# Performance work log

Measured on AMD Instinct MI355X. Metric: run time of the kernel, lower is better.

The kernel has to match this reference:

```python
import jax, jax.numpy as jnp
import numpy as np

NUM_SITES = 64
PHYS_DIM = 2
BOND_DIM = 32
BATCH = 65536


def _build_mps(num_sites, phys_dim, bond_dim, seed=0):
    """Replicates ImprovedMPS._initialize_tensors + _canonical_form, then
    zero-pads ragged cores into a dense [S, D, p, D] stack."""
    rng = np.random.default_rng(seed)
    tensors = []
    cur = 1
    for i in range(num_sites):
        if i == 0:
            nb = min(bond_dim, phys_dim)
            shape = (1, phys_dim, nb)
            cur = nb
        elif i == num_sites - 1:
            shape = (cur, phys_dim, 1)
        else:
            nb = min(bond_dim, cur * phys_dim)
            shape = (cur, phys_dim, nb)
            cur = nb
        ld, rd = shape[0] * shape[1], shape[2]
        m = (rng.standard_normal((ld, rd)) * 0.1).astype(np.float32)
        if ld >= rd:
            q, _ = np.linalg.qr(m)
            t = q.reshape(shape)
        else:
            q, _ = np.linalg.qr(m.T)
            t = q.T.reshape(shape)
        tensors.append(t.astype(np.float32))
    # left-canonical sweep
    for i in range(num_sites - 1):
        l, p, r = tensors[i].shape
        q, rr = np.linalg.qr(tensors[i].reshape(l * p, r))
        tensors[i] = q.reshape(l, p, q.shape[1]).astype(np.float32)
        nl, npd, nr = tensors[i + 1].shape
        tensors[i + 1] = (rr @ tensors[i + 1].reshape(nl, npd * nr)).reshape(rr.shape[0], npd, nr).astype(np.float32)
    # zero-pad ragged bonds into dense stack [S, D, p, D]
    A = np.zeros((num_sites, bond_dim, phys_dim, bond_dim), dtype=np.float32)
    for i, t in enumerate(tensors):
        l, p, r = t.shape
        A[i, :l, :, :r] = t
    return A


def setup_inputs() -> dict:
    key = jax.random.key(0)
    x_batch = jax.random.normal(key, (BATCH, NUM_SITES, PHYS_DIM), dtype=jnp.float32)
    A = jnp.asarray(_build_mps(NUM_SITES, PHYS_DIM, BOND_DIM))
    return {"x_batch": x_batch, "A": A}


def reference(x_batch, A):
    # x_batch: [B, S, p]; A: [S, D, p, D] (zero-padded ragged MPS cores)
    B = x_batch.shape[0]
    D = A.shape[1]
    # left_vector starts as ones(B,1) in the ragged view == one-hot e0 in padded view
    left0 = jnp.zeros((B, D), dtype=x_batch.dtype).at[:, 0].set(1.0)
    xs = jnp.moveaxis(x_batch, 1, 0)  # [S, B, p]

    def step(left, inp):
        A_i, x_i = inp  # [D, p, D], [B, p]
        # fuses: contracted = einsum('bp,lpd->bld'); left = einsum('bl,bld->bd')
        left = jnp.einsum('bl,bp,lpd->bd', left, x_i, A_i)
        return left, None

    left, _ = jax.lax.scan(step, left0, (A, xs))
    return left[:, :1]  # last core has right bond 1 -> only col 0 is nonzero
```

## Files before the change

kernel.cpp:

```cpp
#include <hip/hip_runtime.h>


typedef _Float16 h2 __attribute__((ext_vector_type(2)));
typedef _Float16 half8 __attribute__((ext_vector_type(8)));
typedef float floatx4 __attribute__((ext_vector_type(4)));
typedef float f32x4 __attribute__((ext_vector_type(4)));

#define NPAIRS 32
#define CHUNK_ELEMS 16384

__global__ void mps_prep_pair(const float* __restrict__ A, _Float16* __restrict__ Gf) {
    __shared__ float sA0[2048], sA1[2048], sG[4096];
    const int P = blockIdx.x, tid = threadIdx.x;
    const float* a0p = A + (size_t)(2 * P) * 2048;
    const float* a1p = A + (size_t)(2 * P + 1) * 2048;
#pragma unroll
    for (int i = 0; i < 8; ++i) {
        sA0[tid + 256 * i] = a0p[tid + 256 * i];
        sA1[tid + 256 * i] = a1p[tid + 256 * i];
    }
    __syncthreads();
    {
        const int l = tid >> 3, pq = (tid >> 1) & 3, dh16 = (tid & 1) * 16;
        const int p = pq >> 1, q = pq & 1;
        float accv[16];
#pragma unroll
        for (int dd = 0; dd < 16; ++dd) accv[dd] = 0.f;
        for (int m = 0; m < 32; ++m) {
            const float av = sA0[l * 64 + p * 32 + m];
            const float* bp = &sA1[m * 64 + q * 32 + dh16];
#pragma unroll
            for (int dd = 0; dd < 16; ++dd) accv[dd] += av * bp[dd];
        }
#pragma unroll
        for (int dd = 0; dd < 16; ++dd) sG[l * 128 + pq * 32 + dh16 + dd] = accv[dd];
    }
    __syncthreads();
    const int lane = tid & 63, g = lane >> 4;
#pragma unroll
    for (int pass = 0; pass < 2; ++pass) {
        const int fr = (tid >> 6) + pass * 4;
        const int dh = fr >> 2, kh = fr & 3;
        const int d  = 16 * dh + (lane & 15);
        half8 v;
#pragma unroll
        for (int e = 0; e < 8; ++e) {
            const int l = 4 * g + (e & 3) + 16 * (e >> 2);
            v[e] = (_Float16)sG[l * 128 + kh * 32 + d];
        }
        reinterpret_cast<half8*>(Gf)[((size_t)P * 8 + fr) * 64 + lane] = v;
    }
}

static __device__ __forceinline__ half8 H8(h2 a, h2 b, h2 c, h2 d) {
    half8 r;
    r[0] = a[0]; r[1] = a[1]; r[2] = b[0]; r[3] = b[1];
    r[4] = c[0]; r[5] = c[1]; r[6] = d[0]; r[7] = d[1];
    return r;
}

#define MF(A_, B_, C_) __builtin_amdgcn_mfma_f32_16x16x32_f16(A_, B_, C_, 0, 0, 0)

#define UB(U0, U1, U2, U3, AH0, AH1, XV)                                      \
    {                                                                         \
        h2 b0, b1, b2, b3, w0, w1, w2, w3;                                    \
        b0[0] = (_Float16)AH0[0]; b0[1] = (_Float16)AH0[1];                   \
        b1[0] = (_Float16)AH0[2]; b1[1] = (_Float16)AH0[3];                   \
        b2[0] = (_Float16)AH1[0]; b2[1] = (_Float16)AH1[1];                   \
        b3[0] = (_Float16)AH1[2]; b3[1] = (_Float16)AH1[3];                   \
        _Float16 t_;                                                          \
        t_ = (_Float16)(XV[0] * XV[2]); w0[0] = t_; w0[1] = t_;               \
        t_ = (_Float16)(XV[0] * XV[3]); w1[0] = t_; w1[1] = t_;               \
        t_ = (_Float16)(XV[1] * XV[2]); w2[0] = t_; w2[1] = t_;               \
        t_ = (_Float16)(XV[1] * XV[3]); w3[0] = t_; w3[1] = t_;               \
        U0 = H8(b0 * w0, b1 * w0, b2 * w0, b3 * w0);                          \
        U1 = H8(b0 * w1, b1 * w1, b2 * w1, b3 * w1);                          \
        U2 = H8(b0 * w2, b1 * w2, b2 * w2, b3 * w2);                          \
        U3 = H8(b0 * w3, b1 * w3, b2 * w3, b3 * w3);                          \
    }

#define PAIR(G, I00, I01, I10, I11, O00, O01, O10, O11, XV0, XV1)             \
    {                                                                         \
        half8 u0_, u1_, u2_, u3_, v0_, v1_, v2_, v3_;                         \
        UB(u0_, u1_, u2_, u3_, I00, I01, XV0)                                 \
        UB(v0_, v1_, v2_, v3_, I10, I11, XV1)                                 \
        O00 = MF(G[0], u0_, zv);  O01 = MF(G[4], u0_, zv);                    \
        O10 = MF(G[0], v0_, zv);  O11 = MF(G[4], v0_, zv);                    \
        O00 = MF(G[1], u1_, O00); O01 = MF(G[5], u1_, O01);                   \
        O10 = MF(G[1], v1_, O10); O11 = MF(G[5], v1_, O11);                   \
        O00 = MF(G[2], u2_, O00); O01 = MF(G[6], u2_, O01);                   \
        O10 = MF(G[2], v2_, O10); O11 = MF(G[6], v2_, O11);                   \
        O00 = MF(G[3], u3_, O00); O01 = MF(G[7], u3_, O01);                   \
        O10 = MF(G[3], v3_, O10); O11 = MF(G[7], v3_, O11);                   \
    }

#define RD(DST, BUF, PL)                                                      \
    {                                                                         \
        _Pragma("unroll")                                                     \
        for (int f_ = 0; f_ < 8; ++f_)                                        \
            DST[f_] = *(const half8*)&smA[(BUF) * CHUNK_ELEMS                 \
                                          + (((PL) * 8 + f_) * 64 + lane) * 8]; \
    }

#define STAGE(C, BUF)                                                         \
    {                                                                         \
        _Pragma("unroll")                                                     \
        for (int r_ = 0; r_ < 8; ++r_) {                                      \
            const int rec_ = r_ * 4 + wid;                                    \
            const _Float16* g_ = Gf + (size_t)(C) * CHUNK_ELEMS               \
                                 + rec_ * 512 + lane * 8;                     \
            __builtin_amdgcn_global_load_lds(                                 \
                (const __attribute__((address_space(1))) void*)g_,            \
                (__attribute__((address_space(3))) void*)&smA[(BUF) * CHUNK_ELEMS + rec_ * 512], \
                16, 0, 0);                                                    \
        }                                                                     \
    }

#define CHUNKB(C, BUF, XC0, XC1, XN0, XN1)                                    \
    {                                                                         \
        if ((C) < 7) {                                                        \
            STAGE((C) + 1, 1 - (BUF));                                        \
            _Pragma("unroll")                                                 \
            for (int pp_ = 0; pp_ < 4; ++pp_) {                               \
                XN0[pp_] = xp0[4 * ((C) + 1) + pp_];                          \
                XN1[pp_] = xp1[4 * ((C) + 1) + pp_];                          \
            }                                                                 \
        }                                                                     \
        RD(GB, BUF, 1)                                                        \
        PAIR(GA, p0, p1, q0, q1, np0, np1, nq0, nq1, XC0[0], XC1[0])          \
        RD(GA, BUF, 2)                                                        \
        PAIR(GB, np0, np1, nq0, nq1, p0, p1, q0, q1, XC0[1], XC1[1])          \
        RD(GB, BUF, 3)                                                        \
        PAIR(GA, p0, p1, q0, q1, np0, np1, nq0, nq1, XC0[2], XC1[2])          \
        PAIR(GB, np0, np1, nq0, nq1, p0, p1, q0, q1, XC0[3], XC1[3])          \
        __syncthreads();                                                      \
        if ((C) < 7) RD(GA, 1 - (BUF), 0)                                     \
    }

__global__ __launch_bounds__(256, 2) void mps_main(const float* __restrict__ x,
                                                   const _Float16* __restrict__ Gf,
                                                   float* __restrict__ out) {
    __shared__ __align__(16) _Float16 smA[2 * CHUNK_ELEMS];

    const int lane  = threadIdx.x & 63;
    const int wid   = threadIdx.x >> 6;
    const int wbase = (blockIdx.x * 4 + wid) * 32;
    const int r     = lane & 15;
    const int b0    = wbase + r;
    const int b1    = wbase + 16 + r;

    const f32x4* xp0 = reinterpret_cast<const f32x4*>(x + (size_t)b0 * 128);
    const f32x4* xp1 = reinterpret_cast<const f32x4*>(x + (size_t)b1 * 128);

    floatx4 zv;
#pragma unroll
    for (int i = 0; i < 4; ++i) zv[i] = 0.f;

    floatx4 p0, p1, q0, q1, np0, np1, nq0, nq1;
#pragma unroll
    for (int i = 0; i < 4; ++i) {
        p0[i] = 0.f; p1[i] = 0.f; q0[i] = 0.f; q1[i] = 0.f;
        np0[i] = 0.f; np1[i] = 0.f; nq0[i] = 0.f; nq1[i] = 0.f;
    }
    if (lane < 16) { p0[0] = 1.f; q0[0] = 1.f; }

    f32x4 xa0[4], xa1[4], xb0[4], xb1[4];
    half8 GA[8], GB[8];

    STAGE(0, 0);
#pragma unroll
    for (int pp = 0; pp < 4; ++pp) { xa0[pp] = xp0[pp]; xa1[pp] = xp1[pp]; }
    __syncthreads();
    RD(GA, 0, 0)

    for (int it = 0; it < 4; ++it) {
        const int c0 = 2 * it;
        CHUNKB(c0,     0, xa0, xa1, xb0, xb1)
        CHUNKB(c0 + 1, 1, xb0, xb1, xa0, xa1)
    }

    if (lane < 16) {
        out[wbase + lane]      = p0[0];
        out[wbase + 16 + lane] = q0[0];
    }
}

extern "C" void kernel_launch(void* const* d_in, const int* in_sizes, int n_in,
                              void* d_out, int out_size, void* d_ws, size_t ws_size,
                              hipStream_t stream) {
    const float* x = (const float*)d_in[0];
    const float* A = (const float*)d_in[1];
    float* outp = (float*)d_out;
    _Float16* Gf = (_Float16*)d_ws;

    hipLaunchKernelGGL(mps_prep_pair, dim3(NPAIRS), dim3(256), 0, stream, A, Gf);
    hipLaunchKernelGGL(mps_main, dim3(65536 / 128), dim3(256), 0, stream, x, Gf, outp);
}
```

Baseline: 31.87 us.

## Process four 16-sample tiles per wave with two-wave blocks

```diff
diff --git a/kernel.cpp b/kernel.cpp
--- a/kernel.cpp
+++ b/kernel.cpp
@@ -39,16 +39,24 @@
     const int lane = tid & 63, g = lane >> 4;
 #pragma unroll
     for (int pass = 0; pass < 2; ++pass) {
-        const int fr = (tid >> 6) + pass * 4;
-        const int dh = fr >> 2, kh = fr & 3;
-        const int d  = 16 * dh + (lane & 15);
-        half8 v;
-#pragma unroll
-        for (int e = 0; e < 8; ++e) {
-            const int l = 4 * g + (e & 3) + 16 * (e >> 2);
-            v[e] = (_Float16)sG[l * 128 + kh * 32 + d];
+        const int fr = (tid >> 6) + pass * 2;
+        (void)fr;
+    }
+    {
+        const int lane2 = tid & 63, g2 = lane2 >> 4;
+#pragma unroll
+        for (int pass = 0; pass < 2; ++pass) {
+            const int fr = (tid >> 6) + pass * 4;
+            const int dh = fr >> 2, kh = fr & 3;
+            const int d  = 16 * dh + (lane2 & 15);
+            half8 v;
+#pragma unroll
+            for (int e = 0; e < 8; ++e) {
+                const int l = 4 * g2 + (e & 3) + 16 * (e >> 2);
+                v[e] = (_Float16)sG[l * 128 + kh * 32 + d];
+            }
+            reinterpret_cast<half8*>(Gf)[((size_t)P * 8 + fr) * 64 + lane2] = v;
         }
-        reinterpret_cast<half8*>(Gf)[((size_t)P * 8 + fr) * 64 + lane] = v;
     }
 }
 
@@ -79,20 +87,26 @@
         U3 = H8(b0 * w3, b1 * w3, b2 * w3, b3 * w3);                          \
     }
 
-#define PAIR(G, I00, I01, I10, I11, O00, O01, O10, O11, XV0, XV1)             \
-    {                                                                         \
-        half8 u0_, u1_, u2_, u3_, v0_, v1_, v2_, v3_;                         \
-        UB(u0_, u1_, u2_, u3_, I00, I01, XV0)                                 \
-        UB(v0_, v1_, v2_, v3_, I10, I11, XV1)                                 \
-        O00 = MF(G[0], u0_, zv);  O01 = MF(G[4], u0_, zv);                    \
-        O10 = MF(G[0], v0_, zv);  O11 = MF(G[4], v0_, zv);                    \
-        O00 = MF(G[1], u1_, O00); O01 = MF(G[5], u1_, O01);                   \
-        O10 = MF(G[1], v1_, O10); O11 = MF(G[5], v1_, O11);                   \
-        O00 = MF(G[2], u2_, O00); O01 = MF(G[6], u2_, O01);                   \
-        O10 = MF(G[2], v2_, O10); O11 = MF(G[6], v2_, O11);                   \
-        O00 = MF(G[3], u3_, O00); O01 = MF(G[7], u3_, O01);                   \
-        O10 = MF(G[3], v3_, O10); O11 = MF(G[7], v3_, O11);                   \
-    }
+#define PAIR1(G, I0, I1, O0, O1, XV)                                          \
+    {                                                                         \
+        half8 u0_, u1_, u2_, u3_;                                             \
+        UB(u0_, u1_, u2_, u3_, I0, I1, XV)                                    \
+        O0 = MF(G[0], u0_, zv);  O1 = MF(G[4], u0_, zv);                      \
+        O0 = MF(G[1], u1_, O0);  O1 = MF(G[5], u1_, O1);                      \
+        O0 = MF(G[2], u2_, O0);  O1 = MF(G[6], u2_, O1);                      \
+        O0 = MF(G[3], u3_, O0);  O1 = MF(G[7], u3_, O1);                      \
+    }
+
+#define PAIR4_E(G, XC, PP)                                                    \
+    PAIR1(G, a0h0, a0h1, n0h0, n0h1, XC[0][PP])                               \
+    PAIR1(G, a1h0, a1h1, n1h0, n1h1, XC[1][PP])                               \
+    PAIR1(G, a2h0, a2h1, n2h0, n2h1, XC[2][PP])                               \
+    PAIR1(G, a3h0, a3h1, n3h0, n3h1, XC[3][PP])
+#define PAIR4_O(G, XC, PP)                                                    \
+    PAIR1(G, n0h0, n0h1, a0h0, a0h1, XC[0][PP])                               \
+    PAIR1(G, n1h0, n1h1, a1h0, a1h1, XC[1][PP])                               \
+    PAIR1(G, n2h0, n2h1, a2h0, a2h1, XC[2][PP])                               \
+    PAIR1(G, n3h0, n3h1, a3h0, a3h1, XC[3][PP])
 
 #define RD(DST, BUF, PL)                                                      \
     {                                                                         \
@@ -105,8 +119,8 @@
 #define STAGE(C, BUF)                                                         \
     {                                                                         \
         _Pragma("unroll")                                                     \
-        for (int r_ = 0; r_ < 8; ++r_) {                                      \
-            const int rec_ = r_ * 4 + wid;                                    \
+        for (int r_ = 0; r_ < 16; ++r_) {                                     \
+            const int rec_ = r_ * 2 + wid;                                    \
             const _Float16* g_ = Gf + (size_t)(C) * CHUNK_ELEMS               \
                                  + rec_ * 512 + lane * 8;                     \
             __builtin_amdgcn_global_load_lds(                                 \
@@ -116,72 +130,82 @@
         }                                                                     \
     }
 
-#define CHUNKB(C, BUF, XC0, XC1, XN0, XN1)                                    \
+#define CHUNKB(C, BUF, XC, XN)                                                \
     {                                                                         \
         if ((C) < 7) {                                                        \
             STAGE((C) + 1, 1 - (BUF));                                        \
             _Pragma("unroll")                                                 \
-            for (int pp_ = 0; pp_ < 4; ++pp_) {                               \
-                XN0[pp_] = xp0[4 * ((C) + 1) + pp_];                          \
-                XN1[pp_] = xp1[4 * ((C) + 1) + pp_];                          \
-            }                                                                 \
+            for (int tt_ = 0; tt_ < 4; ++tt_)                                 \
+                _Pragma("unroll")                                             \
+                for (int pp_ = 0; pp_ < 4; ++pp_)                             \
+                    XN[tt_][pp_] = xp[tt_][4 * ((C) + 1) + pp_];              \
         }                                                                     \
         RD(GB, BUF, 1)                                                        \
-        PAIR(GA, p0, p1, q0, q1, np0, np1, nq0, nq1, XC0[0], XC1[0])          \
+        PAIR4_E(GA, XC, 0)                                                    \
         RD(GA, BUF, 2)                                                        \
-        PAIR(GB, np0, np1, nq0, nq1, p0, p1, q0, q1, XC0[1], XC1[1])          \
+        PAIR4_O(GB, XC, 1)                                                    \
         RD(GB, BUF, 3)                                                        \
-        PAIR(GA, p0, p1, q0, q1, np0, np1, nq0, nq1, XC0[2], XC1[2])          \
-        PAIR(GB, np0, np1, nq0, nq1, p0, p1, q0, q1, XC0[3], XC1[3])          \
+        PAIR4_E(GA, XC, 2)                                                    \
+        PAIR4_O(GB, XC, 3)                                                    \
         __syncthreads();                                                      \
         if ((C) < 7) RD(GA, 1 - (BUF), 0)                                     \
     }
 
-__global__ __launch_bounds__(256, 2) void mps_main(const float* __restrict__ x,
+__global__ __launch_bounds__(128, 1) void mps_main(const float* __restrict__ x,
                                                    const _Float16* __restrict__ Gf,
                                                    float* __restrict__ out) {
     __shared__ __align__(16) _Float16 smA[2 * CHUNK_ELEMS];
 
     const int lane  = threadIdx.x & 63;
     const int wid   = threadIdx.x >> 6;
-    const int wbase = (blockIdx.x * 4 + wid) * 32;
+    const int wbase = (blockIdx.x * 2 + wid) * 64;
     const int r     = lane & 15;
-    const int b0    = wbase + r;
-    const int b1    = wbase + 16 + r;
-
-    const f32x4* xp0 = reinterpret_cast<const f32x4*>(x + (size_t)b0 * 128);
-    const f32x4* xp1 = reinterpret_cast<const f32x4*>(x + (size_t)b1 * 128);
+
+    const f32x4* xp[4];
+#pragma unroll
+    for (int tt = 0; tt < 4; ++tt)
+        xp[tt] = reinterpret_cast<const f32x4*>(x + (size_t)(wbase + 16 * tt + r) * 128);
 
     floatx4 zv;
 #pragma unroll
     for (int i = 0; i < 4; ++i) zv[i] = 0.f;
 
-    floatx4 p0, p1, q0, q1, np0, np1, nq0, nq1;
+    floatx4 a0h0, a0h1, a1h0, a1h1, a2h0, a2h1, a3h0, a3h1;
+    floatx4 n0h0, n0h1, n1h0, n1h1, n2h0, n2h1, n3h0, n3h1;
 #pragma unroll
     for (int i = 0; i < 4; ++i) {
-        p0[i] = 0.f; p1[i] = 0.f; q0[i] = 0.f; q1[i] = 0.f;
-        np0[i] = 0.f; np1[i] = 0.f; nq0[i] = 0.f; nq1[i] = 0.f;
-    }
-    if (lane < 16) { p0[0] = 1.f; q0[0] = 1.f; }
-
-    f32x4 xa0[4], xa1[4], xb0[4], xb1[4];
+        a0h0[i] = a0h1[i] = a1h0[i] = a1h1[i] = 0.f;
+        a2h0[i] = a2h1[i] = a3h0[i] = a3h1[i] = 0.f;
+        n0h0[i] = n0h1[i] = n1h0[i] = n1h1[i] = 0.f;
+        n2h0[i] = n2h1[i] = n3h0[i] = n3h1[i] = 0.f;
+    }
+    if (lane < 16) { a0h0[0] = 1.f; a1h0[0] = 1.f; a2h0[0] = 1.f; a3h0[0] = 1.f; }
+
+    f32x4 xa[4][4], xb[4][4];
     half8 GA[8], GB[8];
 
     STAGE(0, 0);
 #pragma unroll
-    for (int pp = 0; pp < 4; ++pp) { xa0[pp] = xp0[pp]; xa1[pp] = xp1[pp]; }
+    for (int tt = 0; tt < 4; ++tt)
+#pragma unroll
+        for (int pp = 0; pp < 4; ++pp) xa[tt][pp] = xp[tt][pp];
     __syncthreads();
     RD(GA, 0, 0)
 
-    for (int it = 0; it < 4; ++it) {
-        const int c0 = 2 * it;
-        CHUNKB(c0,     0, xa0, xa1, xb0, xb1)
-        CHUNKB(c0 + 1, 1, xb0, xb1, xa0, xa1)
-    }
+    CHUNKB(0, 0, xa, xb)
+    CHUNKB(1, 1, xb, xa)
+    CHUNKB(2, 0, xa, xb)
+    CHUNKB(3, 1, xb, xa)
+    CHUNKB(4, 0, xa, xb)
+    CHUNKB(5, 1, xb, xa)
+    CHUNKB(6, 0, xa, xb)
+    CHUNKB(7, 1, xb, xa)
 
     if (lane < 16) {
-        out[wbase + lane]      = p0[0];
-        out[wbase + 16 + lane] = q0[0];
+        out[wbase + lane]      = a0h0[0];
+        out[wbase + 16 + lane] = a1h0[0];
+        out[wbase + 32 + lane] = a2h0[0];
+        out[wbase + 48 + lane] = a3h0[0];
     }
 }
 
@@ -194,5 +218,5 @@
     _Float16* Gf = (_Float16*)d_ws;
 
     hipLaunchKernelGGL(mps_prep_pair, dim3(NPAIRS), dim3(256), 0, stream, A, Gf);
-    hipLaunchKernelGGL(mps_main, dim3(65536 / 128), dim3(256), 0, stream, x, Gf, outp);
-}
+    hipLaunchKernelGGL(mps_main, dim3(65536 / 128), dim3(128), 0, stream, x, Gf, outp);
+}
```

Result: slower. 37.31 us (+17.1%).

## Switch MPS chain to 32x32x16 MFMA with accumulator reused as operand

Applied to the files above, without the earlier changes.

```diff
diff --git a/kernel.cpp b/kernel.cpp
--- a/kernel.cpp
+++ b/kernel.cpp
@@ -1,9 +1,8 @@
 #include <hip/hip_runtime.h>
 
 
-typedef _Float16 h2 __attribute__((ext_vector_type(2)));
 typedef _Float16 half8 __attribute__((ext_vector_type(8)));
-typedef float floatx4 __attribute__((ext_vector_type(4)));
+typedef float floatx16 __attribute__((ext_vector_type(16)));
 typedef float f32x4 __attribute__((ext_vector_type(4)));
 
 #define NPAIRS 32
@@ -36,62 +35,50 @@
         for (int dd = 0; dd < 16; ++dd) sG[l * 128 + pq * 32 + dh16 + dd] = accv[dd];
     }
     __syncthreads();
-    const int lane = tid & 63, g = lane >> 4;
+    const int lane = tid & 63;
+    const int h    = lane >> 5;
+    const int d    = lane & 31;
 #pragma unroll
     for (int pass = 0; pass < 2; ++pass) {
-        const int fr = (tid >> 6) + pass * 4;
-        const int dh = fr >> 2, kh = fr & 3;
-        const int d  = 16 * dh + (lane & 15);
+        const int kf = (tid >> 6) + pass * 4;
+        const int pq = kf >> 1, lh = kf & 1;
         half8 v;
 #pragma unroll
         for (int e = 0; e < 8; ++e) {
-            const int l = 4 * g + (e & 3) + 16 * (e >> 2);
-            v[e] = (_Float16)sG[l * 128 + kh * 32 + d];
+            const int l = 16 * lh + (e & 3) + 8 * (e >> 2) + 4 * h;
+            v[e] = (_Float16)sG[l * 128 + pq * 32 + d];
         }
-        reinterpret_cast<half8*>(Gf)[((size_t)P * 8 + fr) * 64 + lane] = v;
+        reinterpret_cast<half8*>(Gf)[((size_t)P * 8 + kf) * 64 + lane] = v;
     }
 }
 
-static __device__ __forceinline__ half8 H8(h2 a, h2 b, h2 c, h2 d) {
-    half8 r;
-    r[0] = a[0]; r[1] = a[1]; r[2] = b[0]; r[3] = b[1];
-    r[4] = c[0]; r[5] = c[1]; r[6] = d[0]; r[7] = d[1];
-    return r;
-}
+#define MF32(A_, B_, C_) __builtin_amdgcn_mfma_f32_32x32x16_f16(A_, B_, C_, 0, 0, 0)
 
-#define MF(A_, B_, C_) __builtin_amdgcn_mfma_f32_16x16x32_f16(A_, B_, C_, 0, 0, 0)
-
-#define UB(U0, U1, U2, U3, AH0, AH1, XV)                                      \
+#define PAIR1(G, CIN, COUT, XV)                                               \
     {                                                                         \
-        h2 b0, b1, b2, b3, w0, w1, w2, w3;                                    \
-        b0[0] = (_Float16)AH0[0]; b0[1] = (_Float16)AH0[1];                   \
-        b1[0] = (_Float16)AH0[2]; b1[1] = (_Float16)AH0[3];                   \
-        b2[0] = (_Float16)AH1[0]; b2[1] = (_Float16)AH1[1];                   \
-        b3[0] = (_Float16)AH1[2]; b3[1] = (_Float16)AH1[3];                   \
-        _Float16 t_;                                                          \
-        t_ = (_Float16)(XV[0] * XV[2]); w0[0] = t_; w0[1] = t_;               \
-        t_ = (_Float16)(XV[0] * XV[3]); w1[0] = t_; w1[1] = t_;               \
-        t_ = (_Float16)(XV[1] * XV[2]); w2[0] = t_; w2[1] = t_;               \
-        t_ = (_Float16)(XV[1] * XV[3]); w3[0] = t_; w3[1] = t_;               \
-        U0 = H8(b0 * w0, b1 * w0, b2 * w0, b3 * w0);                          \
-        U1 = H8(b0 * w1, b1 * w1, b2 * w1, b3 * w1);                          \
-        U2 = H8(b0 * w2, b1 * w2, b2 * w2, b3 * w2);                          \
-        U3 = H8(b0 * w3, b1 * w3, b2 * w3, b3 * w3);                          \
-    }
-
-#define PAIR(G, I00, I01, I10, I11, O00, O01, O10, O11, XV0, XV1)             \
-    {                                                                         \
-        half8 u0_, u1_, u2_, u3_, v0_, v1_, v2_, v3_;                         \
-        UB(u0_, u1_, u2_, u3_, I00, I01, XV0)                                 \
-        UB(v0_, v1_, v2_, v3_, I10, I11, XV1)                                 \
-        O00 = MF(G[0], u0_, zv);  O01 = MF(G[4], u0_, zv);                    \
-        O10 = MF(G[0], v0_, zv);  O11 = MF(G[4], v0_, zv);                    \
-        O00 = MF(G[1], u1_, O00); O01 = MF(G[5], u1_, O01);                   \
-        O10 = MF(G[1], v1_, O10); O11 = MF(G[5], v1_, O11);                   \
-        O00 = MF(G[2], u2_, O00); O01 = MF(G[6], u2_, O01);                   \
-        O10 = MF(G[2], v2_, O10); O11 = MF(G[6], v2_, O11);                   \
-        O00 = MF(G[3], u3_, O00); O01 = MF(G[7], u3_, O01);                   \
-        O10 = MF(G[3], v3_, O10); O11 = MF(G[7], v3_, O11);                   \
+        half8 FA0_, FA1_;                                                     \
+        _Pragma("unroll")                                                     \
+        for (int i_ = 0; i_ < 8; ++i_) {                                      \
+            FA0_[i_] = (_Float16)CIN[i_];                                     \
+            FA1_[i_] = (_Float16)CIN[8 + i_];                                 \
+        }                                                                     \
+        const _Float16 w0_ = (_Float16)(XV[0] * XV[2]);                       \
+        const _Float16 w1_ = (_Float16)(XV[0] * XV[3]);                       \
+        const _Float16 w2_ = (_Float16)(XV[1] * XV[2]);                       \
+        const _Float16 w3_ = (_Float16)(XV[1] * XV[3]);                       \
+        half8 W0_, W1_, W2_, W3_;                                             \
+        _Pragma("unroll")                                                     \
+        for (int i_ = 0; i_ < 8; ++i_) {                                      \
+            W0_[i_] = w0_; W1_[i_] = w1_; W2_[i_] = w2_; W3_[i_] = w3_;       \
+        }                                                                     \
+        COUT = MF32(G[0], FA0_ * W0_, zv);                                    \
+        COUT = MF32(G[1], FA1_ * W0_, COUT);                                  \
+        COUT = MF32(G[2], FA0_ * W1_, COUT);                                  \
+        COUT = MF32(G[3], FA1_ * W1_, COUT);                                  \
+        COUT = MF32(G[4], FA0_ * W2_, COUT);                                  \
+        COUT = MF32(G[5], FA1_ * W2_, COUT);                                  \
+        COUT = MF32(G[6], FA0_ * W3_, COUT);                                  \
+        COUT = MF32(G[7], FA1_ * W3_, COUT);                                  \
     }
 
 #define RD(DST, BUF, PL)                                                      \
@@ -105,8 +92,8 @@
 #define STAGE(C, BUF)                                                         \
     {                                                                         \
         _Pragma("unroll")                                                     \
-        for (int r_ = 0; r_ < 8; ++r_) {                                      \
-            const int rec_ = r_ * 4 + wid;                                    \
+        for (int r_ = 0; r_ < 16; ++r_) {                                     \
+            const int rec_ = r_ * 2 + wid;                                    \
             const _Float16* g_ = Gf + (size_t)(C) * CHUNK_ELEMS               \
                                  + rec_ * 512 + lane * 8;                     \
             __builtin_amdgcn_global_load_lds(                                 \
@@ -116,7 +103,7 @@
         }                                                                     \
     }
 
-#define CHUNKB(C, BUF, XC0, XC1, XN0, XN1)                                    \
+#define CHUNKB(C, BUF, XT0, XT1, XN0, XN1)                                    \
     {                                                                         \
         if ((C) < 7) {                                                        \
             STAGE((C) + 1, 1 - (BUF));                                        \
@@ -127,42 +114,41 @@
             }                                                                 \
         }                                                                     \
         RD(GB, BUF, 1)                                                        \
-        PAIR(GA, p0, p1, q0, q1, np0, np1, nq0, nq1, XC0[0], XC1[0])          \
+        PAIR1(GA, c0, d0, XT0[0])                                             \
+        PAIR1(GA, c1, d1, XT1[0])                                             \
         RD(GA, BUF, 2)                                                        \
-        PAIR(GB, np0, np1, nq0, nq1, p0, p1, q0, q1, XC0[1], XC1[1])          \
+        PAIR1(GB, d0, c0, XT0[1])                                             \
+        PAIR1(GB, d1, c1, XT1[1])                                             \
         RD(GB, BUF, 3)                                                        \
-        PAIR(GA, p0, p1, q0, q1, np0, np1, nq0, nq1, XC0[2], XC1[2])          \
-        PAIR(GB, np0, np1, nq0, nq1, p0, p1, q0, q1, XC0[3], XC1[3])          \
+        PAIR1(GA, c0, d0, XT0[2])                                             \
+        PAIR1(GA, c1, d1, XT1[2])                                             \
+        PAIR1(GB, d0, c0, XT0[3])                                             \
+        PAIR1(GB, d1, c1, XT1[3])                                             \
         __syncthreads();                                                      \
         if ((C) < 7) RD(GA, 1 - (BUF), 0)                                     \
     }
 
-__global__ __launch_bounds__(256, 2) void mps_main(const float* __restrict__ x,
+__global__ __launch_bounds__(128, 1) void mps_main(const float* __restrict__ x,
                                                    const _Float16* __restrict__ Gf,
                                                    float* __restrict__ out) {
     __shared__ __align__(16) _Float16 smA[2 * CHUNK_ELEMS];
 
     const int lane  = threadIdx.x & 63;
     const int wid   = threadIdx.x >> 6;
-    const int wbase = (blockIdx.x * 4 + wid) * 32;
-    const int r     = lane & 15;
-    const int b0    = wbase + r;
-    const int b1    = wbase + 16 + r;
+    const int wbase = (blockIdx.x * 2 + wid) * 64;
+    const int col   = lane & 31;
 
-    const f32x4* xp0 = reinterpret_cast<const f32x4*>(x + (size_t)b0 * 128);
-    const f32x4* xp1 = reinterpret_cast<const f32x4*>(x + (size_t)b1 * 128);
+    const f32x4* xp0 = reinterpret_cast<const f32x4*>(x + (size_t)(wbase + col) * 128);
+    const f32x4* xp1 = reinterpret_cast<const f32x4*>(x + (size_t)(wbase + 32 + col) * 128);
 
-    floatx4 zv;
+    floatx16 zv;
 #pragma unroll
-    for (int i = 0; i < 4; ++i) zv[i] = 0.f;
+    for (int i = 0; i < 16; ++i) zv[i] = 0.f;
 
-    floatx4 p0, p1, q0, q1, np0, np1, nq0, nq1;
+    floatx16 c0, c1, d0, d1;
 #pragma unroll
-    for (int i = 0; i < 4; ++i) {
-        p0[i] = 0.f; p1[i] = 0.f; q0[i] = 0.f; q1[i] = 0.f;
-        np0[i] = 0.f; np1[i] = 0.f; nq0[i] = 0.f; nq1[i] = 0.f;
-    }
-    if (lane < 16) { p0[0] = 1.f; q0[0] = 1.f; }
+    for (int i = 0; i < 16; ++i) { c0[i] = 0.f; c1[i] = 0.f; d0[i] = 0.f; d1[i] = 0.f; }
+    if (lane < 32) { c0[0] = 1.f; c1[0] = 1.f; }
 
     f32x4 xa0[4], xa1[4], xb0[4], xb1[4];
     half8 GA[8], GB[8];
@@ -173,15 +159,18 @@
     __syncthreads();
     RD(GA, 0, 0)
 
-    for (int it = 0; it < 4; ++it) {
-        const int c0 = 2 * it;
-        CHUNKB(c0,     0, xa0, xa1, xb0, xb1)
-        CHUNKB(c0 + 1, 1, xb0, xb1, xa0, xa1)
-    }
+    CHUNKB(0, 0, xa0, xa1, xb0, xb1)
+    CHUNKB(1, 1, xb0, xb1, xa0, xa1)
+    CHUNKB(2, 0, xa0, xa1, xb0, xb1)
+    CHUNKB(3, 1, xb0, xb1, xa0, xa1)
+    CHUNKB(4, 0, xa0, xa1, xb0, xb1)
+    CHUNKB(5, 1, xb0, xb1, xa0, xa1)
+    CHUNKB(6, 0, xa0, xa1, xb0, xb1)
+    CHUNKB(7, 1, xb0, xb1, xa0, xa1)
 
-    if (lane < 16) {
-        out[wbase + lane]      = p0[0];
-        out[wbase + 16 + lane] = q0[0];
+    if (lane < 32) {
+        out[wbase + lane]      = c0[0];
+        out[wbase + 32 + lane] = c1[0];
     }
 }
 
@@ -194,5 +183,5 @@
     _Float16* Gf = (_Float16*)d_ws;
 
     hipLaunchKernelGGL(mps_prep_pair, dim3(NPAIRS), dim3(256), 0, stream, A, Gf);
-    hipLaunchKernelGGL(mps_main, dim3(65536 / 128), dim3(256), 0, stream, x, Gf, outp);
+    hipLaunchKernelGGL(mps_main, dim3(65536 / 128), dim3(128), 0, stream, x, Gf, outp);
 }
```

Measured after the change: 29.24 us. -8.2%, faster.
